# Kernel optimization log

Hardware: AMD Instinct MI355X
Metric: run time of the kernel (lower is better)

Reference implementation:

```python
import jax, jax.numpy as jnp
import numpy as np

B, S, T, H, NH, NL = 16, 128, 64, 128, 8, 4
DH = H // NH
FF = 2 * H
SCALE = 1.0 / float(np.sqrt(DH))


def _ln(x, s, b):
    m = x.mean(-1, keepdims=True)
    v = ((x - m) ** 2).mean(-1, keepdims=True)
    return (x - m) * jax.lax.rsqrt(v + 1e-5) * s + b


def _block(x, mask, p):
    Wq, bq, Wk, bk, Wv, bv, Wo, bo, s1, c1, W1, d1, W2, d2, s2, c2 = p
    N, L, _ = x.shape
    q = (x @ Wq + bq).reshape(N, L, NH, DH)
    k = (x @ Wk + bk).reshape(N, L, NH, DH)
    v = (x @ Wv + bv).reshape(N, L, NH, DH)
    scores = jnp.einsum('nqhd,nkhd->nhqk', q, k) * SCALE
    scores = jnp.where(mask[:, None, :, :], scores, -1e9)
    a = jax.nn.softmax(scores, axis=-1)
    o = jnp.einsum('nhqk,nkhd->nqhd', a, v).reshape(N, L, H)
    x = _ln(x + o @ Wo + bo, s1, c1)
    h = jax.nn.relu(x @ W1 + d1)
    return _ln(x + h @ W2 + d2, s2, c2)


def setup_inputs():
    key = jax.random.key(0)
    ks = jax.random.split(key, 16)
    g = lambda k, shape: jax.random.normal(k, shape, jnp.float32) * 0.02
    return {
        'polylines': jax.random.normal(ks[0], (B, S, T, H), jnp.float32),
        'lengths': jax.random.randint(ks[1], (B, S), 0, T + 1),
        'proj_w': g(ks[2], (H, H)), 'proj_b': jnp.zeros((H,), jnp.float32),
        'proj_ln_s': jnp.ones((H,), jnp.float32), 'proj_ln_b': jnp.zeros((H,), jnp.float32),
        'pos_emb': g(ks[3], (1, T, H)),
        'Wq': g(ks[4], (NL, H, H)), 'bq': jnp.zeros((NL, H), jnp.float32),
        'Wk': g(ks[5], (NL, H, H)), 'bk': jnp.zeros((NL, H), jnp.float32),
        'Wv': g(ks[6], (NL, H, H)), 'bv': jnp.zeros((NL, H), jnp.float32),
        'Wo': g(ks[7], (NL, H, H)), 'bo': jnp.zeros((NL, H), jnp.float32),
        'ln1_s': jnp.ones((NL, H), jnp.float32), 'ln1_b': jnp.zeros((NL, H), jnp.float32),
        'W1': g(ks[8], (NL, H, FF)), 'b1': jnp.zeros((NL, FF), jnp.float32),
        'W2': g(ks[9], (NL, FF, H)), 'b2': jnp.zeros((NL, H), jnp.float32),
        'ln2_s': jnp.ones((NL, H), jnp.float32), 'ln2_b': jnp.zeros((NL, H), jnp.float32),
    }


def reference(polylines, lengths, proj_w, proj_b, proj_ln_s, proj_ln_b, pos_emb,
              Wq, bq, Wk, bk, Wv, bv, Wo, bo, ln1_s, ln1_b, W1, b1, W2, b2, ln2_s, ln2_b):
    # valid[b,s,t] = t < lengths[b,s]; lengths==0 -> polyline absent (fully padded)
    valid = jnp.arange(T)[None, None, :] < lengths[:, :, None]  # [B,S,T]
    x = jnp.where(valid[..., None], polylines, -1.0)            # -1 pad as in np.pad(constant_values=-1)
    # mask_temporal[b,s] = outer(valid[b,s], valid[b,s])
    mask_t = (valid[:, :, :, None] & valid[:, :, None, :]).reshape(B * S, T, T)
    # mask_spatial[b,t] = outer(valid[b,:,t], valid[b,:,t])
    vs = jnp.transpose(valid, (0, 2, 1))                        # [B,T,S]
    mask_s = (vs[:, :, :, None] & vs[:, :, None, :]).reshape(B * T, S, S)

    x = x.reshape(B * S, T, H)
    x = jax.nn.relu(_ln(x @ proj_w + proj_b, proj_ln_s, proj_ln_b))  # MLP: Linear->LN->ReLU
    x = x + pos_emb[:, :T, :]

    mask = mask_t
    for i in range(NL):
        if i == NL // 2:
            # switch from temporal to spatial attention: [B*S,T,H] -> [B*T,S,H]
            x = x.reshape(B, S, T, H).transpose(0, 2, 1, 3).reshape(B * T, S, H)
            mask = mask_s
        p = (Wq[i], bq[i], Wk[i], bk[i], Wv[i], bv[i], Wo[i], bo[i],
             ln1_s[i], ln1_b[i], W1[i], b1[i], W2[i], b2[i], ln2_s[i], ln2_b[i])
        x = _block(x, mask, p)
    # faithful to original final reshape (treats [B*T,S,H] buffer as [B,S,T,H])
    return x.reshape(B, S, T, H)[:, 0, :]
```

## Files before the change

kernel.cpp:

```cpp
#include <hip/hip_runtime.h>

typedef short short8 __attribute__((ext_vector_type(8)));
typedef short short4_t __attribute__((ext_vector_type(4)));
typedef float floatx4 __attribute__((ext_vector_type(4)));
typedef unsigned short ushort_t;

#define B_ 16
#define S_ 128
#define T_ 64
#define H_ 128
#define FF_ 256
#define SCALEQK 0.25f

#define OFFP 0
#define OFFQ(l) (16384 + (l) * 65536)
#define OFFK(l) (OFFQ(l) + 16384)
#define OFFV(l) (OFFQ(l) + 32768)
#define OFFO(l) (OFFQ(l) + 49152)
#define OFFW1(l) (278528 + (l) * 65536)
#define OFFW2(l) (OFFW1(l) + 32768)

__device__ __forceinline__ float b2f(ushort_t u) {
    union { unsigned int i; float f; } x; x.i = ((unsigned int)u) << 16; return x.f;
}
__device__ __forceinline__ ushort_t f2b(float f) {
    union { float f; unsigned int i; } x; x.f = f;
    unsigned int r = x.i + 0x7fffu + ((x.i >> 16) & 1u);
    return (ushort_t)(r >> 16);
}
__device__ __forceinline__ int pack2b(float a, float b) {
    return (int)f2b(a) | ((int)f2b(b) << 16);
}

struct WtEnt { const float* src; int N; int K; int nclog2; int dstoff; };
struct WtArgs { WtEnt e[25]; };

__global__ __launch_bounds__(256) void wt_kernel(WtArgs a, ushort_t* __restrict__ dst) {
    WtEnt ent = a.e[blockIdx.x];
    const int tiles_c = ent.N >> 5;
    const int nt = (ent.K >> 5) * tiles_c;
    const int t = blockIdx.y;
    if (t >= nt) return;
    const int tc = t & (tiles_c - 1);
    const int tr = t >> ent.nclog2;
    __shared__ float ld[32 * 33];
    const int tid = threadIdx.x;
#pragma unroll
    for (int i = 0; i < 4; ++i) {
        int e = tid + i * 256;
        int rr = e >> 5, cc = e & 31;
        ld[rr * 33 + cc] = ent.src[(tr * 32 + rr) * ent.N + tc * 32 + cc];
    }
    __syncthreads();
    ushort_t* d = dst + ent.dstoff;
#pragma unroll
    for (int i = 0; i < 4; ++i) {
        int e = tid + i * 256;
        int rr = e >> 5, cc = e & 31;
        d[(tc * 32 + rr) * ent.K + tr * 32 + cc] = f2b(ld[cc * 33 + rr]);
    }
}

template<int RT, int CT, int KK>
__device__ __forceinline__ void mm_g(const ushort_t* aL, int sa,
                                     const ushort_t* __restrict__ wT,
                                     int colbase, int lane, floatx4 (&acc)[RT][CT]) {
    const int l15 = lane & 15, lq8 = (lane >> 4) * 8;
#pragma unroll
    for (int r = 0; r < RT; ++r)
#pragma unroll
        for (int c = 0; c < CT; ++c) acc[r][c] = (floatx4){0.f, 0.f, 0.f, 0.f};
#pragma unroll
    for (int k0 = 0; k0 < KK; k0 += 32) {
        short8 b[CT];
#pragma unroll
        for (int c = 0; c < CT; ++c)
            b[c] = *(const short8*)&wT[(colbase + c * 16 + l15) * KK + k0 + lq8];
#pragma unroll
        for (int r = 0; r < RT; ++r) {
            short8 a = *(const short8*)&aL[(r * 16 + l15) * sa + k0 + lq8];
#pragma unroll
            for (int c = 0; c < CT; ++c)
                acc[r][c] = __builtin_amdgcn_mfma_f32_16x16x32_bf16(a, b[c], acc[r][c], 0, 0, 0);
        }
    }
}

template<int RT, int CT>
__device__ __forceinline__ void add_bias(floatx4 (&acc)[RT][CT], const float* b,
                                         int colbase, int l15) {
#pragma unroll
    for (int c = 0; c < CT; ++c) {
        float bc = b[colbase + c * 16 + l15];
#pragma unroll
        for (int r = 0; r < RT; ++r)
#pragma unroll
            for (int g = 0; g < 4; ++g) acc[r][c][g] += bc;
    }
}

template<int RT, int CT>
__device__ __forceinline__ void add_resid_reg(floatx4 (&acc)[RT][CT],
                                              const float (&res)[RT][CT][4]) {
#pragma unroll
    for (int r = 0; r < RT; ++r)
#pragma unroll
        for (int c = 0; c < CT; ++c)
#pragma unroll
            for (int g = 0; g < 4; ++g) acc[r][c][g] += res[r][c][g];
}
template<int RT, int CT>
__device__ __forceinline__ void save_resid(float (&res)[RT][CT][4],
                                           const floatx4 (&acc)[RT][CT]) {
#pragma unroll
    for (int r = 0; r < RT; ++r)
#pragma unroll
        for (int c = 0; c < CT; ++c)
#pragma unroll
            for (int g = 0; g < 4; ++g) res[r][c][g] = acc[r][c][g];
}

template<int RT, int CT>
__device__ __forceinline__ void st_n(const floatx4 (&acc)[RT][CT], ushort_t* dst, int stride,
                                     int colbase, int l15, int lq) {
#pragma unroll
    for (int r = 0; r < RT; ++r)
#pragma unroll
        for (int g = 0; g < 4; ++g) {
            int row = r * 16 + lq * 4 + g;
#pragma unroll
            for (int c = 0; c < CT; ++c)
                dst[row * stride + colbase + c * 16 + l15] = f2b(acc[r][c][g]);
        }
}

template<int RT, int CT>
__device__ __forceinline__ void st_t(const floatx4 (&acc)[RT][CT], ushort_t* dst, int stride,
                                     int colbase, int l15, int lq) {
#pragma unroll
    for (int r = 0; r < RT; ++r)
#pragma unroll
        for (int c = 0; c < CT; ++c) {
            int d = colbase + c * 16 + l15;
            short4_t p;
#pragma unroll
            for (int g = 0; g < 4; ++g) p[g] = (short)f2b(acc[r][c][g]);
            *(short4_t*)&dst[d * stride + r * 16 + lq * 4] = p;
        }
}

template<int RT, int CT>
__device__ __forceinline__ void ln_norm(floatx4 (&acc)[RT][CT], float* redL,
                                        const float* lns, const float* lnb,
                                        int colbase, int l15, int lq, int wv) {
#pragma unroll
    for (int r = 0; r < RT; ++r)
#pragma unroll
        for (int g = 0; g < 4; ++g) {
            float s = 0.f, q = 0.f;
#pragma unroll
            for (int c = 0; c < CT; ++c) { float v = acc[r][c][g]; s += v; q += v * v; }
            s += __shfl_xor(s, 1); s += __shfl_xor(s, 2); s += __shfl_xor(s, 4); s += __shfl_xor(s, 8);
            q += __shfl_xor(q, 1); q += __shfl_xor(q, 2); q += __shfl_xor(q, 4); q += __shfl_xor(q, 8);
            if (l15 == 0) {
                int row = r * 16 + lq * 4 + g;
                redL[row * 8 + wv] = s;
                redL[row * 8 + 4 + wv] = q;
            }
        }
    __syncthreads();
#pragma unroll
    for (int r = 0; r < RT; ++r)
#pragma unroll
        for (int g = 0; g < 4; ++g) {
            int row = r * 16 + lq * 4 + g;
            float4 S = *(float4*)&redL[row * 8];
            float4 Q = *(float4*)&redL[row * 8 + 4];
            float mean = (S.x + S.y + S.z + S.w) * (1.f / 128.f);
            float var = (Q.x + Q.y + Q.z + Q.w) * (1.f / 128.f) - mean * mean;
            float rstd = rsqrtf(var + 1e-5f);
#pragma unroll
            for (int c = 0; c < CT; ++c) {
                int col = colbase + c * 16 + l15;
                acc[r][c][g] = (acc[r][c][g] - mean) * rstd * lns[col] + lnb[col];
            }
        }
}

template<int JT>
__device__ __forceinline__ void softmax_pack(floatx4 (&st)[JT], bool iv, unsigned jm,
                                             int (&px)[JT][2]) {
    float ev[JT][4];
    float mx = -3.0e38f;
#pragma unroll
    for (int jt = 0; jt < JT; ++jt)
#pragma unroll
        for (int g = 0; g < 4; ++g) {
            bool ok = iv && ((jm >> (jt * 4 + g)) & 1u);
            float s = ok ? st[jt][g] * SCALEQK : -1e9f;
            ev[jt][g] = s; mx = fmaxf(mx, s);
        }
    mx = fmaxf(mx, __shfl_xor(mx, 16)); mx = fmaxf(mx, __shfl_xor(mx, 32));
    float sum = 0.f;
#pragma unroll
    for (int jt = 0; jt < JT; ++jt)
#pragma unroll
        for (int g = 0; g < 4; ++g) { float e = __expf(ev[jt][g] - mx); ev[jt][g] = e; sum += e; }
    sum += __shfl_xor(sum, 16); sum += __shfl_xor(sum, 32);
    float inv = 1.f / sum;
#pragma unroll
    for (int jt = 0; jt < JT; ++jt) {
        px[jt][0] = pack2b(ev[jt][0] * inv, ev[jt][1] * inv);
        px[jt][1] = pack2b(ev[jt][2] * inv, ev[jt][3] * inv);
    }
}

__device__ __forceinline__ short8 pfrag(const int (*px)[2], int jc, int lq, int l15) {
    const int jA = (lq & 1) * 32 + l15;
    int a0 = __shfl(px[jc * 2][0], jA);
    int a1 = __shfl(px[jc * 2][1], jA);
    int a2 = __shfl(px[jc * 2][0], jA + 16);
    int a3 = __shfl(px[jc * 2][1], jA + 16);
    int b0 = __shfl(px[jc * 2 + 1][0], jA);
    int b1 = __shfl(px[jc * 2 + 1][1], jA);
    int b2 = __shfl(px[jc * 2 + 1][0], jA + 16);
    int b3 = __shfl(px[jc * 2 + 1][1], jA + 16);
    const bool t = (lq >> 1) != 0;
    union { int4 i; short8 s; } u;
    u.i = make_int4(t ? b0 : a0, t ? b1 : a1, t ? b2 : a2, t ? b3 : a3);
    return u.s;
}
__device__ __forceinline__ short8 vfrag(const ushort_t* vT, int stride, int row, int off) {
    int2 a = *(const int2*)&vT[row * stride + off];
    int2 b = *(const int2*)&vT[row * stride + off + 4];
    union { int4 i; short8 s; } u;
    u.i = make_int4(a.x, a.y, b.x, b.y);
    return u.s;
}

__global__ __launch_bounds__(256, 2) void k1_mega(
    const float* __restrict__ poly, const int* __restrict__ lens,
    const ushort_t* __restrict__ wt,
    const float* __restrict__ projb, const float* __restrict__ pls,
    const float* __restrict__ plb, const float* __restrict__ pos,
    const float* __restrict__ bq0, const float* __restrict__ bk0,
    const float* __restrict__ bv0, const float* __restrict__ bo0,
    const float* __restrict__ l1s0, const float* __restrict__ l1b0,
    const float* __restrict__ b10, const float* __restrict__ b20,
    const float* __restrict__ l2s0, const float* __restrict__ l2b0,
    const float* __restrict__ bq1, const float* __restrict__ bk1,
    const float* __restrict__ bv1,
    ushort_t* __restrict__ o1, float* __restrict__ xr0f)
{
    __shared__ ushort_t pool[34816];
    __shared__ float redL[512];
    __shared__ float psL[8 * 68];
    __shared__ float q1L[128];
    ushort_t* xL = pool;
    ushort_t* qL = pool + 8704;
    ushort_t* kL = pool + 17408;
    ushort_t* vT = pool + 26112;
    ushort_t* hL = pool + 17408;

    const int tid = threadIdx.x, lane = tid & 63, wv = tid >> 6;
    const int l15 = lane & 15, lq = lane >> 4;
    const int g = blockIdx.x;
    const int len = lens[g];

    {
        const float* pg = poly + (size_t)g * 8192;
#pragma unroll
        for (int it = 0; it < 8; ++it) {
            int e4 = (tid + it * 256) * 4;
            int row = e4 >> 7, col = e4 & 127;
            float4 f = *(const float4*)(pg + e4);
            if (row >= len) { f.x = -1.f; f.y = -1.f; f.z = -1.f; f.w = -1.f; }
            short4_t u;
            u[0] = (short)f2b(f.x); u[1] = (short)f2b(f.y);
            u[2] = (short)f2b(f.z); u[3] = (short)f2b(f.w);
            *(short4_t*)&xL[row * 136 + col] = u;
        }
    }
    __syncthreads();

    floatx4 a2[4][2];
    float xre[4][2][4];

    mm_g<4, 2, 128>(xL, 136, wt + OFFP, wv * 32, lane, a2);
    add_bias<4, 2>(a2, projb, wv * 32, l15);
    ln_norm<4, 2>(a2, redL, pls, plb, wv * 32, l15, lq, wv);
    __syncthreads();
#pragma unroll
    for (int r = 0; r < 4; ++r)
#pragma unroll
        for (int gg = 0; gg < 4; ++gg) {
            int row = r * 16 + lq * 4 + gg;
#pragma unroll
            for (int c = 0; c < 2; ++c) {
                int col = wv * 32 + c * 16 + l15;
                float v = fmaxf(a2[r][c][gg], 0.f) + pos[row * 128 + col];
                xre[r][c][gg] = v;
                xL[row * 136 + col] = f2b(v);
            }
        }
    __syncthreads();

    mm_g<4, 2, 128>(xL, 136, wt + OFFQ(0), wv * 32, lane, a2);
    add_bias<4, 2>(a2, bq0, wv * 32, l15);
    st_n<4, 2>(a2, qL, 136, wv * 32, l15, lq);
    mm_g<4, 2, 128>(xL, 136, wt + OFFK(0), wv * 32, lane, a2);
    add_bias<4, 2>(a2, bk0, wv * 32, l15);
    st_n<4, 2>(a2, kL, 136, wv * 32, l15, lq);
    mm_g<4, 2, 128>(xL, 136, wt + OFFV(0), wv * 32, lane, a2);
    add_bias<4, 2>(a2, bv0, wv * 32, l15);
    st_t<4, 2>(a2, vT, 68, wv * 32, l15, lq);
    __syncthreads();

    {
        const int iRow = wv * 16 + l15;
        const bool iv = iRow < len;
        unsigned jm = 0;
#pragma unroll
        for (int jt = 0; jt < 4; ++jt)
#pragma unroll
            for (int gg = 0; gg < 4; ++gg)
                if (jt * 16 + lq * 4 + gg < len) jm |= (1u << (jt * 4 + gg));
        for (int h = 0; h < 8; ++h) {
            const int hc = h * 16;
            short8 z8 = {0, 0, 0, 0, 0, 0, 0, 0};
            short8 bqf = z8;
            if (lq < 2) bqf = *(const short8*)&qL[iRow * 136 + hc + lq * 8];
            floatx4 st[4];
#pragma unroll
            for (int jt = 0; jt < 4; ++jt) {
                short8 ak = z8;
                if (lq < 2) ak = *(const short8*)&kL[(jt * 16 + l15) * 136 + hc + lq * 8];
                floatx4 zz = {0.f, 0.f, 0.f, 0.f};
                st[jt] = __builtin_amdgcn_mfma_f32_16x16x32_bf16(ak, bqf, zz, 0, 0, 0);
            }
            int px[4][2];
            softmax_pack<4>(st, iv, jm, px);
            floatx4 ao = {0.f, 0.f, 0.f, 0.f};
#pragma unroll
            for (int jc = 0; jc < 2; ++jc) {
                short8 av = vfrag(vT, 68, hc + l15, jc * 32 + lq * 8);
                short8 bp = pfrag(px, jc, lq, l15);
                ao = __builtin_amdgcn_mfma_f32_16x16x32_bf16(av, bp, ao, 0, 0, 0);
            }
            short4_t w;
#pragma unroll
            for (int gg = 0; gg < 4; ++gg) w[gg] = (short)f2b(ao[gg]);
            *(short4_t*)&qL[iRow * 136 + hc + lq * 4] = w;
        }
    }
    __syncthreads();

    mm_g<4, 2, 128>(qL, 136, wt + OFFO(0), wv * 32, lane, a2);
    add_bias<4, 2>(a2, bo0, wv * 32, l15);
    add_resid_reg<4, 2>(a2, xre);
    ln_norm<4, 2>(a2, redL, l1s0, l1b0, wv * 32, l15, lq, wv);
    save_resid<4, 2>(xre, a2);
    st_n<4, 2>(a2, xL, 136, wv * 32, l15, lq);
    __syncthreads();

    {
        floatx4 a4[4][4];
        mm_g<4, 4, 128>(xL, 136, wt + OFFW1(0), wv * 64, lane, a4);
        add_bias<4, 4>(a4, b10, wv * 64, l15);
#pragma unroll
        for (int r = 0; r < 4; ++r)
#pragma unroll
            for (int c = 0; c < 4; ++c)
#pragma unroll
                for (int gg = 0; gg < 4; ++gg) a4[r][c][gg] = fmaxf(a4[r][c][gg], 0.f);
        st_n<4, 4>(a4, hL, 272, wv * 64, l15, lq);
    }
    __syncthreads();

    mm_g<4, 2, 256>(hL, 272, wt + OFFW2(0), wv * 32, lane, a2);
    add_bias<4, 2>(a2, b20, wv * 32, l15);
    add_resid_reg<4, 2>(a2, xre);
    ln_norm<4, 2>(a2, redL, l2s0, l2b0, wv * 32, l15, lq, wv);
    save_resid<4, 2>(xre, a2);
    st_n<4, 2>(a2, xL, 136, wv * 32, l15, lq);
    if (lq == 0) {
#pragma unroll
        for (int c = 0; c < 2; ++c)
            xr0f[(size_t)g * 128 + wv * 32 + c * 16 + l15] = a2[0][c][0];
    }
    __syncthreads();

    mm_g<4, 2, 128>(xL, 136, wt + OFFK(1), wv * 32, lane, a2);
    add_bias<4, 2>(a2, bk1, wv * 32, l15);
    st_n<4, 2>(a2, kL, 136, wv * 32, l15, lq);
    mm_g<4, 2, 128>(xL, 136, wt + OFFV(1), wv * 32, lane, a2);
    add_bias<4, 2>(a2, bv1, wv * 32, l15);
    st_t<4, 2>(a2, vT, 68, wv * 32, l15, lq);
    if (tid < 128) {
        int d = tid;
        float a = bq1[d];
        const ushort_t* wq = wt + OFFQ(1) + d * 128;
#pragma unroll 4
        for (int j0 = 0; j0 < 128; j0 += 8) {
            short8 w8 = *(const short8*)&wq[j0];
            short8 x8 = *(const short8*)&xL[j0];
#pragma unroll
            for (int q = 0; q < 8; ++q)
                a = fmaf(b2f((ushort_t)x8[q]), b2f((ushort_t)w8[q]), a);
        }
        q1L[d] = a;
    }
    __syncthreads();

    {
        int h = tid >> 5, jj = tid & 31;
        int hc = h * 16;
        float s[2];
#pragma unroll
        for (int half = 0; half < 2; ++half) {
            int j = jj + half * 32;
            float a = 0.f;
            short8 k0v = *(const short8*)&kL[j * 136 + hc];
            short8 k1v = *(const short8*)&kL[j * 136 + hc + 8];
#pragma unroll
            for (int q = 0; q < 8; ++q) {
                a = fmaf(q1L[hc + q], b2f((ushort_t)k0v[q]), a);
                a = fmaf(q1L[hc + 8 + q], b2f((ushort_t)k1v[q]), a);
            }
            s[half] = (j < len) ? a * SCALEQK : -1e9f;
        }
        float mx = fmaxf(s[0], s[1]);
#pragma unroll
        for (int d = 1; d < 32; d <<= 1) mx = fmaxf(mx, __shfl_xor(mx, d));
        float e0 = __expf(s[0] - mx), e1 = __expf(s[1] - mx);
        float sum = e0 + e1;
#pragma unroll
        for (int d = 1; d < 32; d <<= 1) sum += __shfl_xor(sum, d);
        float inv = 1.f / sum;
        psL[h * 68 + jj] = e0 * inv;
        psL[h * 68 + jj + 32] = e1 * inv;
    }
    __syncthreads();
    if (tid < 128) {
        int h = tid >> 4, d = tid & 15, hc = h * 16;
        float a = 0.f;
#pragma unroll 4
        for (int j0 = 0; j0 < 64; j0 += 4) {
            float4 p4 = *(const float4*)&psL[h * 68 + j0];
            short4_t v4 = *(const short4_t*)&vT[(hc + d) * 68 + j0];
            a += p4.x * b2f((ushort_t)v4[0]) + p4.y * b2f((ushort_t)v4[1])
               + p4.z * b2f((ushort_t)v4[2]) + p4.w * b2f((ushort_t)v4[3]);
        }
        o1[(size_t)g * 128 + hc + d] = f2b(a);
    }
}

__global__ __launch_bounds__(256, 1) void k2_tail(
    const int* __restrict__ lens, const ushort_t* __restrict__ wt,
    const ushort_t* __restrict__ o1, const float* __restrict__ xr0f,
    const float* __restrict__ bq, const float* __restrict__ bk,
    const float* __restrict__ bv, const float* __restrict__ bo,
    const float* __restrict__ l1s, const float* __restrict__ l1b,
    const float* __restrict__ b1, const float* __restrict__ b2,
    const float* __restrict__ l2s, const float* __restrict__ l2b,
    float* __restrict__ outp)
{
    __shared__ ushort_t pool[69632];
    __shared__ float redL[1024];
    __shared__ int vld[128];
    ushort_t* yL = pool;
    ushort_t* qL = pool + 17408;
    ushort_t* kL = pool + 34816;
    ushort_t* vT = pool + 52224;
    ushort_t* hL = pool + 34816;

    const int tid = threadIdx.x, lane = tid & 63, wv = tid >> 6;
    const int l15 = lane & 15, lq = lane >> 4;
    const int b = blockIdx.x;

    if (tid < 128) vld[tid] = (lens[b * 128 + tid] > 0) ? 1 : 0;
#pragma unroll
    for (int it = 0; it < 8; ++it) {
        int e = tid + it * 256;
        int row = e >> 4, cg = e & 15;
        *(short8*)&kL[row * 136 + cg * 8] =
            *(const short8*)&o1[((size_t)b * 128 + row) * 128 + cg * 8];
    }
    __syncthreads();

    floatx4 a2[8][2];
    float yre[8][2][4];

    mm_g<8, 2, 128>(kL, 136, wt + OFFO(1), wv * 32, lane, a2);
    add_bias<8, 2>(a2, bo + 128, wv * 32, l15);
#pragma unroll
    for (int r = 0; r < 8; ++r)
#pragma unroll
        for (int gg = 0; gg < 4; ++gg) {
            int row = r * 16 + lq * 4 + gg;
#pragma unroll
            for (int c = 0; c < 2; ++c)
                a2[r][c][gg] += xr0f[((size_t)b * 128 + row) * 128 + wv * 32 + c * 16 + l15];
        }
    ln_norm<8, 2>(a2, redL, l1s + 128, l1b + 128, wv * 32, l15, lq, wv);
    save_resid<8, 2>(yre, a2);
    st_n<8, 2>(a2, yL, 136, wv * 32, l15, lq);
    __syncthreads();
    {
        floatx4 a4[8][4];
        mm_g<8, 4, 128>(yL, 136, wt + OFFW1(1), wv * 64, lane, a4);
        add_bias<8, 4>(a4, b1 + FF_, wv * 64, l15);
#pragma unroll
        for (int r = 0; r < 8; ++r)
#pragma unroll
            for (int c = 0; c < 4; ++c)
#pragma unroll
                for (int gg = 0; gg < 4; ++gg) a4[r][c][gg] = fmaxf(a4[r][c][gg], 0.f);
        st_n<8, 4>(a4, hL, 272, wv * 64, l15, lq);
    }
    __syncthreads();
    mm_g<8, 2, 256>(hL, 272, wt + OFFW2(1), wv * 32, lane, a2);
    add_bias<8, 2>(a2, b2 + 128, wv * 32, l15);
    add_resid_reg<8, 2>(a2, yre);
    ln_norm<8, 2>(a2, redL, l2s + 128, l2b + 128, wv * 32, l15, lq, wv);
    save_resid<8, 2>(yre, a2);
    st_n<8, 2>(a2, yL, 136, wv * 32, l15, lq);
    __syncthreads();

    unsigned jm = 0;
#pragma unroll
    for (int jt = 0; jt < 8; ++jt)
#pragma unroll
        for (int gg = 0; gg < 4; ++gg)
            if (vld[jt * 16 + lq * 4 + gg]) jm |= (1u << (jt * 4 + gg));
    const int i0 = wv * 32 + l15, i1 = i0 + 16;
    const bool iv0 = vld[i0] != 0, iv1 = vld[i1] != 0;

    for (int l = 2; l < 4; ++l) {
        mm_g<8, 2, 128>(yL, 136, wt + OFFQ(l), wv * 32, lane, a2);
        add_bias<8, 2>(a2, bq + l * 128, wv * 32, l15);
        st_n<8, 2>(a2, qL, 136, wv * 32, l15, lq);
        mm_g<8, 2, 128>(yL, 136, wt + OFFK(l), wv * 32, lane, a2);
        add_bias<8, 2>(a2, bk + l * 128, wv * 32, l15);
        st_n<8, 2>(a2, kL, 136, wv * 32, l15, lq);
        mm_g<8, 2, 128>(yL, 136, wt + OFFV(l), wv * 32, lane, a2);
        add_bias<8, 2>(a2, bv + l * 128, wv * 32, l15);
        st_t<8, 2>(a2, vT, 136, wv * 32, l15, lq);
        __syncthreads();
        for (int h = 0; h < 8; ++h) {
            const int hc = h * 16;
            short8 z8 = {0, 0, 0, 0, 0, 0, 0, 0};
            short8 bqa = z8, bqb = z8;
            if (lq < 2) {
                bqa = *(const short8*)&qL[i0 * 136 + hc + lq * 8];
                bqb = *(const short8*)&qL[i1 * 136 + hc + lq * 8];
            }
            floatx4 s0[8], s1[8];
#pragma unroll
            for (int jt = 0; jt < 8; ++jt) {
                short8 ak = z8;
                if (lq < 2) ak = *(const short8*)&kL[(jt * 16 + l15) * 136 + hc + lq * 8];
                floatx4 zz = {0.f, 0.f, 0.f, 0.f};
                s0[jt] = __builtin_amdgcn_mfma_f32_16x16x32_bf16(ak, bqa, zz, 0, 0, 0);
                s1[jt] = __builtin_amdgcn_mfma_f32_16x16x32_bf16(ak, bqb, zz, 0, 0, 0);
            }
            int px0[8][2], px1[8][2];
            softmax_pack<8>(s0, iv0, jm, px0);
            softmax_pack<8>(s1, iv1, jm, px1);
            floatx4 o0 = {0.f, 0.f, 0.f, 0.f}, o1a = {0.f, 0.f, 0.f, 0.f};
#pragma unroll
            for (int jc = 0; jc < 4; ++jc) {
                short8 av = vfrag(vT, 136, hc + l15, jc * 32 + lq * 8);
                o0 = __builtin_amdgcn_mfma_f32_16x16x32_bf16(av, pfrag(px0, jc, lq, l15), o0, 0, 0, 0);
                o1a = __builtin_amdgcn_mfma_f32_16x16x32_bf16(av, pfrag(px1, jc, lq, l15), o1a, 0, 0, 0);
            }
            short4_t w0, w1;
#pragma unroll
            for (int gg = 0; gg < 4; ++gg) { w0[gg] = (short)f2b(o0[gg]); w1[gg] = (short)f2b(o1a[gg]); }
            *(short4_t*)&qL[i0 * 136 + hc + lq * 4] = w0;
            *(short4_t*)&qL[i1 * 136 + hc + lq * 4] = w1;
        }
        __syncthreads();
        mm_g<8, 2, 128>(qL, 136, wt + OFFO(l), wv * 32, lane, a2);
        add_bias<8, 2>(a2, bo + l * 128, wv * 32, l15);
        add_resid_reg<8, 2>(a2, yre);
        ln_norm<8, 2>(a2, redL, l1s + l * 128, l1b + l * 128, wv * 32, l15, lq, wv);
        save_resid<8, 2>(yre, a2);
        st_n<8, 2>(a2, yL, 136, wv * 32, l15, lq);
        __syncthreads();
        {
            floatx4 a4[8][4];
            mm_g<8, 4, 128>(yL, 136, wt + OFFW1(l), wv * 64, lane, a4);
            add_bias<8, 4>(a4, b1 + l * FF_, wv * 64, l15);
#pragma unroll
            for (int r = 0; r < 8; ++r)
#pragma unroll
                for (int c = 0; c < 4; ++c)
#pragma unroll
                    for (int gg = 0; gg < 4; ++gg) a4[r][c][gg] = fmaxf(a4[r][c][gg], 0.f);
            st_n<8, 4>(a4, hL, 272, wv * 64, l15, lq);
        }
        __syncthreads();
        mm_g<8, 2, 256>(hL, 272, wt + OFFW2(l), wv * 32, lane, a2);
        add_bias<8, 2>(a2, b2 + l * 128, wv * 32, l15);
        add_resid_reg<8, 2>(a2, yre);
        ln_norm<8, 2>(a2, redL, l2s + l * 128, l2b + l * 128, wv * 32, l15, lq, wv);
        if (l == 3) {
#pragma unroll
            for (int r = 0; r < 4; ++r)
#pragma unroll
                for (int gg = 0; gg < 4; ++gg) {
                    int row = r * 16 + lq * 4 + gg;
#pragma unroll
                    for (int c = 0; c < 2; ++c)
                        outp[(size_t)b * 8192 + row * 128 + wv * 32 + c * 16 + l15] = a2[r][c][gg];
                }
        } else {
            save_resid<8, 2>(yre, a2);
            st_n<8, 2>(a2, yL, 136, wv * 32, l15, lq);
        }
        __syncthreads();
    }
}

extern "C" void kernel_launch(void* const* d_in, const int* in_sizes, int n_in,
                              void* d_out, int out_size, void* d_ws, size_t ws_size,
                              hipStream_t stream)
{
    const float* poly   = (const float*)d_in[0];
    const int*   lens   = (const int*)d_in[1];
    const float* proj_w = (const float*)d_in[2];
    const float* proj_b = (const float*)d_in[3];
    const float* pls    = (const float*)d_in[4];
    const float* plb    = (const float*)d_in[5];
    const float* pos    = (const float*)d_in[6];
    const float* Wq = (const float*)d_in[7];
    const float* bq = (const float*)d_in[8];
    const float* Wk = (const float*)d_in[9];
    const float* bk = (const float*)d_in[10];
    const float* Wv = (const float*)d_in[11];
    const float* bv = (const float*)d_in[12];
    const float* Wo = (const float*)d_in[13];
    const float* bo = (const float*)d_in[14];
    const float* l1s = (const float*)d_in[15];
    const float* l1b = (const float*)d_in[16];
    const float* W1 = (const float*)d_in[17];
    const float* b1 = (const float*)d_in[18];
    const float* W2 = (const float*)d_in[19];
    const float* b2 = (const float*)d_in[20];
    const float* l2s = (const float*)d_in[21];
    const float* l2b = (const float*)d_in[22];
    float* outp = (float*)d_out;

    char* base = (char*)d_ws;
    ushort_t* wt    = (ushort_t*)base;
    ushort_t* o1buf = (ushort_t*)(base + 1081344);
    float* xr0f     = (float*)(base + 1605632);

    const int HH = H_ * H_, HF = H_ * FF_;
    WtArgs wa;
    wa.e[0] = {proj_w, 128, 128, 2, OFFP};
    for (int l = 0; l < 4; ++l) {
        wa.e[1 + l * 4 + 0] = {Wq + l * HH, 128, 128, 2, OFFQ(l)};
        wa.e[1 + l * 4 + 1] = {Wk + l * HH, 128, 128, 2, OFFK(l)};
        wa.e[1 + l * 4 + 2] = {Wv + l * HH, 128, 128, 2, OFFV(l)};
        wa.e[1 + l * 4 + 3] = {Wo + l * HH, 128, 128, 2, OFFO(l)};
    }
    for (int l = 0; l < 4; ++l) {
        wa.e[17 + l * 2 + 0] = {W1 + l * HF, 256, 128, 3, OFFW1(l)};
        wa.e[17 + l * 2 + 1] = {W2 + l * HF, 128, 256, 2, OFFW2(l)};
    }
    wt_kernel<<<dim3(25, 32), 256, 0, stream>>>(wa, wt);

    k1_mega<<<dim3(2048), 256, 0, stream>>>(
        poly, lens, wt,
        proj_b, pls, plb, pos,
        bq, bk, bv, bo, l1s, l1b, b1, b2, l2s, l2b,
        bq + H_, bk + H_, bv + H_,
        o1buf, xr0f);

    k2_tail<<<dim3(16), 256, 0, stream>>>(
        lens, wt, o1buf, xr0f,
        bq, bk, bv, bo, l1s, l1b, b1, b2, l2s, l2b,
        outp);
}
```

Before: 471.6 us.

## Split fused spatial-attention tail into separate GEMM and attention kernels

Replaces the single 16-block tail kernel, which ran the remaining spatial transformer layers, with a chain of generic MFMA GEMM kernels and a separate scalar attention kernel. Fused epilogues handle bias, ReLU and residual plus layernorm. The goal is to spread the tail work over more blocks, using column and Q/K/V splits and per-head-pair attention blocks. The cost is many extra launches and global-memory round trips for intermediates, and the attention now runs on scalar FMAs instead of MFMA.

```diff
diff --git a/kernel.cpp b/kernel.cpp
--- a/kernel.cpp
+++ b/kernel.cpp
@@ -11,6 +11,11 @@
 #define H_ 128
 #define FF_ 256
 #define SCALEQK 0.25f
+
+#define EPI_BIAS 0
+#define EPI_RELU 1
+#define EPI_LNRES 2
+#define EPI_PROJ 3
 
 #define OFFP 0
 #define OFFQ(l) (16384 + (l) * 65536)
@@ -59,6 +64,240 @@
         int rr = e >> 5, cc = e & 31;
         d[(tc * 32 + rr) * ent.K + tr * 32 + cc] = f2b(ld[cc * 33 + rr]);
     }
+}
+
+template<int K, int EPI, bool PAD, bool FINAL, bool MULTI, bool OUTB, bool AB16>
+__global__ __launch_bounds__(256, 2) void gemm_mfma(
+    const void* __restrict__ Av, int lda,
+    const ushort_t* wt0, const ushort_t* wt1, const ushort_t* wt2,
+    const float* b0, const float* b1, const float* b2,
+    const float* __restrict__ resid, int rstride,
+    const float* __restrict__ lns, const float* __restrict__ lnb,
+    const float* __restrict__ pos, const int* __restrict__ lens,
+    void* o0, void* o1, void* o2,
+    int Ntot)
+{
+    __shared__ ushort_t aL[128 * 136];
+    __shared__ ushort_t wL[128 * 136];
+
+    const int tid = threadIdx.x;
+    const int lane = tid & 63, wv = tid >> 6;
+    const size_t rowbase = (size_t)blockIdx.x * 128;
+
+    const ushort_t* wT; const float* bias; void* out; int cbase;
+    if (MULTI) {
+        int sel = blockIdx.y;
+        wT = sel == 0 ? wt0 : (sel == 1 ? wt1 : wt2);
+        bias = sel == 0 ? b0 : (sel == 1 ? b1 : b2);
+        out = sel == 0 ? o0 : (sel == 1 ? o1 : o2);
+        cbase = 0;
+    } else {
+        wT = wt0; bias = b0; out = o0; cbase = blockIdx.y * 128;
+    }
+
+    floatx4 acc[2][8];
+#pragma unroll
+    for (int a = 0; a < 2; ++a)
+#pragma unroll
+        for (int c = 0; c < 8; ++c) acc[a][c] = (floatx4){0.f, 0.f, 0.f, 0.f};
+
+    const int arow = wv * 32 + (lane & 15);
+    const int koff = (lane >> 4) * 8;
+
+    for (int kc = 0; kc < K; kc += 128) {
+        if (kc) __syncthreads();
+#pragma unroll
+        for (int it = 0; it < 8; ++it) {
+            int e8 = tid + it * 256;
+            int row = e8 >> 4, kg = e8 & 15;
+            int kk = kc + kg * 8;
+            short8 val;
+            if (AB16) {
+                val = *(const short8*)((const ushort_t*)Av + (size_t)(rowbase + row) * lda + kk);
+            } else {
+                const float* Af = (const float*)Av + (size_t)(rowbase + row) * lda + kk;
+                float f[8];
+                *(float4*)(f) = *(const float4*)(Af);
+                *(float4*)(f + 4) = *(const float4*)(Af + 4);
+                if (PAD) {
+                    int r = (int)(rowbase + row);
+                    if ((r & 63) >= lens[r >> 6]) {
+#pragma unroll
+                        for (int q = 0; q < 8; ++q) f[q] = -1.0f;
+                    }
+                }
+#pragma unroll
+                for (int q = 0; q < 8; ++q) val[q] = (short)f2b(f[q]);
+            }
+            *(short8*)&aL[row * 136 + kg * 8] = val;
+        }
+#pragma unroll
+        for (int it = 0; it < 8; ++it) {
+            int e8 = tid + it * 256;
+            int n = e8 >> 4, kg = e8 & 15;
+            *(short8*)&wL[n * 136 + kg * 8] =
+                *(const short8*)&wT[(size_t)(cbase + n) * K + kc + kg * 8];
+        }
+        __syncthreads();
+#pragma unroll
+        for (int k0 = 0; k0 < 128; k0 += 32) {
+            short8 a0 = *(const short8*)&aL[arow * 136 + k0 + koff];
+            short8 a1 = *(const short8*)&aL[(arow + 16) * 136 + k0 + koff];
+#pragma unroll
+            for (int ct = 0; ct < 8; ++ct) {
+                short8 b = *(const short8*)&wL[(ct * 16 + (lane & 15)) * 136 + k0 + koff];
+                acc[0][ct] = __builtin_amdgcn_mfma_f32_16x16x32_bf16(a0, b, acc[0][ct], 0, 0, 0);
+                acc[1][ct] = __builtin_amdgcn_mfma_f32_16x16x32_bf16(a1, b, acc[1][ct], 0, 0, 0);
+            }
+        }
+    }
+
+    const int col16 = lane & 15;
+    const int rgrp = (lane >> 4) * 4;
+    float bcol[8], lnsc[8], lnbc[8];
+#pragma unroll
+    for (int ct = 0; ct < 8; ++ct) bcol[ct] = bias[cbase + ct * 16 + col16];
+    if (EPI == EPI_LNRES || EPI == EPI_PROJ) {
+#pragma unroll
+        for (int ct = 0; ct < 8; ++ct) {
+            lnsc[ct] = lns[ct * 16 + col16];
+            lnbc[ct] = lnb[ct * 16 + col16];
+        }
+    }
+
+#pragma unroll
+    for (int rt = 0; rt < 2; ++rt) {
+        const int rbase = wv * 32 + rt * 16 + rgrp;
+#pragma unroll
+        for (int ct = 0; ct < 8; ++ct)
+#pragma unroll
+            for (int rg = 0; rg < 4; ++rg) {
+                float v = acc[rt][ct][rg] + bcol[ct];
+                if (EPI == EPI_LNRES)
+                    v += resid[(rowbase + rbase + rg) * (size_t)rstride + ct * 16 + col16];
+                acc[rt][ct][rg] = v;
+            }
+        if (EPI == EPI_LNRES || EPI == EPI_PROJ) {
+            float mean[4], rstd[4];
+#pragma unroll
+            for (int rg = 0; rg < 4; ++rg) {
+                float s = 0.f;
+#pragma unroll
+                for (int ct = 0; ct < 8; ++ct) s += acc[rt][ct][rg];
+                s += __shfl_xor(s, 1); s += __shfl_xor(s, 2);
+                s += __shfl_xor(s, 4); s += __shfl_xor(s, 8);
+                mean[rg] = s * (1.f / 128.f);
+            }
+#pragma unroll
+            for (int rg = 0; rg < 4; ++rg) {
+                float s = 0.f;
+#pragma unroll
+                for (int ct = 0; ct < 8; ++ct) {
+                    float d = acc[rt][ct][rg] - mean[rg];
+                    s += d * d;
+                }
+                s += __shfl_xor(s, 1); s += __shfl_xor(s, 2);
+                s += __shfl_xor(s, 4); s += __shfl_xor(s, 8);
+                rstd[rg] = rsqrtf(s * (1.f / 128.f) + 1e-5f);
+            }
+#pragma unroll
+            for (int ct = 0; ct < 8; ++ct)
+#pragma unroll
+                for (int rg = 0; rg < 4; ++rg)
+                    acc[rt][ct][rg] = (acc[rt][ct][rg] - mean[rg]) * rstd[rg] * lnsc[ct] + lnbc[ct];
+        }
+#pragma unroll
+        for (int ct = 0; ct < 8; ++ct)
+#pragma unroll
+            for (int rg = 0; rg < 4; ++rg) {
+                size_t grow = rowbase + rbase + rg;
+                int col = cbase + ct * 16 + col16;
+                float v = acc[rt][ct][rg];
+                if (EPI == EPI_RELU) v = fmaxf(v, 0.f);
+                if (EPI == EPI_PROJ)
+                    v = fmaxf(v, 0.f) + pos[((int)grow & 63) * H_ + ct * 16 + col16];
+                if (FINAL) {
+                    int b = (int)(grow >> 7), s = (int)(grow & 127);
+                    if (s < T_) ((float*)out)[((size_t)(b * T_ + s)) * H_ + col] = v;
+                } else if (OUTB) {
+                    ((ushort_t*)out)[grow * (size_t)Ntot + col] = f2b(v);
+                } else {
+                    ((float*)out)[grow * (size_t)Ntot + col] = v;
+                }
+            }
+    }
+}
+
+__global__ __launch_bounds__(256, 1) void attn_s(
+    ushort_t* qo, const ushort_t* __restrict__ kk, const ushort_t* __restrict__ vv,
+    const int* __restrict__ lens)
+{
+    __shared__ float kL[128 * 36];
+    __shared__ float vL[128 * 36];
+    __shared__ int vldL[128];
+    const int tid = threadIdx.x;
+    const int b = blockIdx.x, hp = blockIdx.y;
+    const size_t rowg = (size_t)b * 128;
+
+    if (tid < 128) vldL[tid] = (lens[b * 128 + tid] > 0) ? 1 : 0;
+#pragma unroll
+    for (int it = 0; it < 2; ++it) {
+        int e8 = tid + it * 256;
+        int j = e8 >> 2, dg = e8 & 3;
+        short8 k8 = *(const short8*)&kk[(rowg + j) * 128 + hp * 32 + dg * 8];
+        short8 v8 = *(const short8*)&vv[(rowg + j) * 128 + hp * 32 + dg * 8];
+        float* kd = &kL[j * 36 + dg * 8];
+        float* vd = &vL[j * 36 + dg * 8];
+#pragma unroll
+        for (int q = 0; q < 8; ++q) { kd[q] = b2f((ushort_t)k8[q]); vd[q] = b2f((ushort_t)v8[q]); }
+    }
+    __syncthreads();
+
+    const int hl = tid >> 7;
+    const int i = tid & 127;
+    const int hc = hl * 16;
+    const int h = hp * 2 + hl;
+
+    float qf[16];
+    {
+        const short8* qp = (const short8*)&qo[(rowg + i) * 128 + h * 16];
+        short8 q0 = qp[0], q1 = qp[1];
+#pragma unroll
+        for (int q = 0; q < 8; ++q) { qf[q] = b2f((ushort_t)q0[q]); qf[8 + q] = b2f((ushort_t)q1[q]); }
+    }
+
+    float sc[128];
+    const bool iv = vldL[i] != 0;
+#pragma unroll
+    for (int j = 0; j < 128; ++j) {
+        const float* kr = &kL[j * 36 + hc];
+        float s = 0.f;
+#pragma unroll
+        for (int d = 0; d < 16; ++d) s = fmaf(qf[d], kr[d], s);
+        sc[j] = (iv && vldL[j]) ? s * SCALEQK : -1e9f;
+    }
+    float m = -3.0e38f;
+#pragma unroll
+    for (int j = 0; j < 128; ++j) m = fmaxf(m, sc[j]);
+    float sum = 0.f;
+#pragma unroll
+    for (int j = 0; j < 128; ++j) { float e = __expf(sc[j] - m); sc[j] = e; sum += e; }
+    const float inv = 1.0f / sum;
+    float of[16];
+#pragma unroll
+    for (int d = 0; d < 16; ++d) of[d] = 0.f;
+#pragma unroll
+    for (int j = 0; j < 128; ++j) {
+        float p = sc[j] * inv;
+        const float* vr = &vL[j * 36 + hc];
+#pragma unroll
+        for (int d = 0; d < 16; ++d) of[d] = fmaf(p, vr[d], of[d]);
+    }
+    short8 o0v, o1v;
+#pragma unroll
+    for (int q = 0; q < 8; ++q) { o0v[q] = (short)f2b(of[q]); o1v[q] = (short)f2b(of[8 + q]); }
+    short8* op = (short8*)&qo[(rowg + i) * 128 + h * 16];
+    op[0] = o0v; op[1] = o1v;
 }
 
 template<int RT, int CT, int KK>
@@ -264,11 +503,11 @@
 
     const int tid = threadIdx.x, lane = tid & 63, wv = tid >> 6;
     const int l15 = lane & 15, lq = lane >> 4;
-    const int g = blockIdx.x;
-    const int len = lens[g];
+    const int gid = blockIdx.x;
+    const int len = lens[gid];
 
     {
-        const float* pg = poly + (size_t)g * 8192;
+        const float* pg = poly + (size_t)gid * 8192;
 #pragma unroll
         for (int it = 0; it < 8; ++it) {
             int e4 = (tid + it * 256) * 4;
@@ -386,7 +625,7 @@
     if (lq == 0) {
 #pragma unroll
         for (int c = 0; c < 2; ++c)
-            xr0f[(size_t)g * 128 + wv * 32 + c * 16 + l15] = a2[0][c][0];
+            xr0f[(size_t)gid * 128 + wv * 32 + c * 16 + l15] = a2[0][c][0];
     }
     __syncthreads();
 
@@ -451,175 +690,7 @@
             a += p4.x * b2f((ushort_t)v4[0]) + p4.y * b2f((ushort_t)v4[1])
                + p4.z * b2f((ushort_t)v4[2]) + p4.w * b2f((ushort_t)v4[3]);
         }
-        o1[(size_t)g * 128 + hc + d] = f2b(a);
-    }
-}
-
-__global__ __launch_bounds__(256, 1) void k2_tail(
-    const int* __restrict__ lens, const ushort_t* __restrict__ wt,
-    const ushort_t* __restrict__ o1, const float* __restrict__ xr0f,
-    const float* __restrict__ bq, const float* __restrict__ bk,
-    const float* __restrict__ bv, const float* __restrict__ bo,
-    const float* __restrict__ l1s, const float* __restrict__ l1b,
-    const float* __restrict__ b1, const float* __restrict__ b2,
-    const float* __restrict__ l2s, const float* __restrict__ l2b,
-    float* __restrict__ outp)
-{
-    __shared__ ushort_t pool[69632];
-    __shared__ float redL[1024];
-    __shared__ int vld[128];
-    ushort_t* yL = pool;
-    ushort_t* qL = pool + 17408;
-    ushort_t* kL = pool + 34816;
-    ushort_t* vT = pool + 52224;
-    ushort_t* hL = pool + 34816;
-
-    const int tid = threadIdx.x, lane = tid & 63, wv = tid >> 6;
-    const int l15 = lane & 15, lq = lane >> 4;
-    const int b = blockIdx.x;
-
-    if (tid < 128) vld[tid] = (lens[b * 128 + tid] > 0) ? 1 : 0;
-#pragma unroll
-    for (int it = 0; it < 8; ++it) {
-        int e = tid + it * 256;
-        int row = e >> 4, cg = e & 15;
-        *(short8*)&kL[row * 136 + cg * 8] =
-            *(const short8*)&o1[((size_t)b * 128 + row) * 128 + cg * 8];
-    }
-    __syncthreads();
-
-    floatx4 a2[8][2];
-    float yre[8][2][4];
-
-    mm_g<8, 2, 128>(kL, 136, wt + OFFO(1), wv * 32, lane, a2);
-    add_bias<8, 2>(a2, bo + 128, wv * 32, l15);
-#pragma unroll
-    for (int r = 0; r < 8; ++r)
-#pragma unroll
-        for (int gg = 0; gg < 4; ++gg) {
-            int row = r * 16 + lq * 4 + gg;
-#pragma unroll
-            for (int c = 0; c < 2; ++c)
-                a2[r][c][gg] += xr0f[((size_t)b * 128 + row) * 128 + wv * 32 + c * 16 + l15];
-        }
-    ln_norm<8, 2>(a2, redL, l1s + 128, l1b + 128, wv * 32, l15, lq, wv);
-    save_resid<8, 2>(yre, a2);
-    st_n<8, 2>(a2, yL, 136, wv * 32, l15, lq);
-    __syncthreads();
-    {
-        floatx4 a4[8][4];
-        mm_g<8, 4, 128>(yL, 136, wt + OFFW1(1), wv * 64, lane, a4);
-        add_bias<8, 4>(a4, b1 + FF_, wv * 64, l15);
-#pragma unroll
-        for (int r = 0; r < 8; ++r)
-#pragma unroll
-            for (int c = 0; c < 4; ++c)
-#pragma unroll
-                for (int gg = 0; gg < 4; ++gg) a4[r][c][gg] = fmaxf(a4[r][c][gg], 0.f);
-        st_n<8, 4>(a4, hL, 272, wv * 64, l15, lq);
-    }
-    __syncthreads();
-    mm_g<8, 2, 256>(hL, 272, wt + OFFW2(1), wv * 32, lane, a2);
-    add_bias<8, 2>(a2, b2 + 128, wv * 32, l15);
-    add_resid_reg<8, 2>(a2, yre);
-    ln_norm<8, 2>(a2, redL, l2s + 128, l2b + 128, wv * 32, l15, lq, wv);
-    save_resid<8, 2>(yre, a2);
-    st_n<8, 2>(a2, yL, 136, wv * 32, l15, lq);
-    __syncthreads();
-
-    unsigned jm = 0;
-#pragma unroll
-    for (int jt = 0; jt < 8; ++jt)
-#pragma unroll
-        for (int gg = 0; gg < 4; ++gg)
-            if (vld[jt * 16 + lq * 4 + gg]) jm |= (1u << (jt * 4 + gg));
-    const int i0 = wv * 32 + l15, i1 = i0 + 16;
-    const bool iv0 = vld[i0] != 0, iv1 = vld[i1] != 0;
-
-    for (int l = 2; l < 4; ++l) {
-        mm_g<8, 2, 128>(yL, 136, wt + OFFQ(l), wv * 32, lane, a2);
-        add_bias<8, 2>(a2, bq + l * 128, wv * 32, l15);
-        st_n<8, 2>(a2, qL, 136, wv * 32, l15, lq);
-        mm_g<8, 2, 128>(yL, 136, wt + OFFK(l), wv * 32, lane, a2);
-        add_bias<8, 2>(a2, bk + l * 128, wv * 32, l15);
-        st_n<8, 2>(a2, kL, 136, wv * 32, l15, lq);
-        mm_g<8, 2, 128>(yL, 136, wt + OFFV(l), wv * 32, lane, a2);
-        add_bias<8, 2>(a2, bv + l * 128, wv * 32, l15);
-        st_t<8, 2>(a2, vT, 136, wv * 32, l15, lq);
-        __syncthreads();
-        for (int h = 0; h < 8; ++h) {
-            const int hc = h * 16;
-            short8 z8 = {0, 0, 0, 0, 0, 0, 0, 0};
-            short8 bqa = z8, bqb = z8;
-            if (lq < 2) {
-                bqa = *(const short8*)&qL[i0 * 136 + hc + lq * 8];
-                bqb = *(const short8*)&qL[i1 * 136 + hc + lq * 8];
-            }
-            floatx4 s0[8], s1[8];
-#pragma unroll
-            for (int jt = 0; jt < 8; ++jt) {
-                short8 ak = z8;
-                if (lq < 2) ak = *(const short8*)&kL[(jt * 16 + l15) * 136 + hc + lq * 8];
-                floatx4 zz = {0.f, 0.f, 0.f, 0.f};
-                s0[jt] = __builtin_amdgcn_mfma_f32_16x16x32_bf16(ak, bqa, zz, 0, 0, 0);
-                s1[jt] = __builtin_amdgcn_mfma_f32_16x16x32_bf16(ak, bqb, zz, 0, 0, 0);
-            }
-            int px0[8][2], px1[8][2];
-            softmax_pack<8>(s0, iv0, jm, px0);
-            softmax_pack<8>(s1, iv1, jm, px1);
-            floatx4 o0 = {0.f, 0.f, 0.f, 0.f}, o1a = {0.f, 0.f, 0.f, 0.f};
-#pragma unroll
-            for (int jc = 0; jc < 4; ++jc) {
-                short8 av = vfrag(vT, 136, hc + l15, jc * 32 + lq * 8);
-                o0 = __builtin_amdgcn_mfma_f32_16x16x32_bf16(av, pfrag(px0, jc, lq, l15), o0, 0, 0, 0);
-                o1a = __builtin_amdgcn_mfma_f32_16x16x32_bf16(av, pfrag(px1, jc, lq, l15), o1a, 0, 0, 0);
-            }
-            short4_t w0, w1;
-#pragma unroll
-            for (int gg = 0; gg < 4; ++gg) { w0[gg] = (short)f2b(o0[gg]); w1[gg] = (short)f2b(o1a[gg]); }
-            *(short4_t*)&qL[i0 * 136 + hc + lq * 4] = w0;
-            *(short4_t*)&qL[i1 * 136 + hc + lq * 4] = w1;
-        }
-        __syncthreads();
-        mm_g<8, 2, 128>(qL, 136, wt + OFFO(l), wv * 32, lane, a2);
-        add_bias<8, 2>(a2, bo + l * 128, wv * 32, l15);
-        add_resid_reg<8, 2>(a2, yre);
-        ln_norm<8, 2>(a2, redL, l1s + l * 128, l1b + l * 128, wv * 32, l15, lq, wv);
-        save_resid<8, 2>(yre, a2);
-        st_n<8, 2>(a2, yL, 136, wv * 32, l15, lq);
-        __syncthreads();
-        {
-            floatx4 a4[8][4];
-            mm_g<8, 4, 128>(yL, 136, wt + OFFW1(l), wv * 64, lane, a4);
-            add_bias<8, 4>(a4, b1 + l * FF_, wv * 64, l15);
-#pragma unroll
-            for (int r = 0; r < 8; ++r)
-#pragma unroll
-                for (int c = 0; c < 4; ++c)
-#pragma unroll
-                    for (int gg = 0; gg < 4; ++gg) a4[r][c][gg] = fmaxf(a4[r][c][gg], 0.f);
-            st_n<8, 4>(a4, hL, 272, wv * 64, l15, lq);
-        }
-        __syncthreads();
-        mm_g<8, 2, 256>(hL, 272, wt + OFFW2(l), wv * 32, lane, a2);
-        add_bias<8, 2>(a2, b2 + l * 128, wv * 32, l15);
-        add_resid_reg<8, 2>(a2, yre);
-        ln_norm<8, 2>(a2, redL, l2s + l * 128, l2b + l * 128, wv * 32, l15, lq, wv);
-        if (l == 3) {
-#pragma unroll
-            for (int r = 0; r < 4; ++r)
-#pragma unroll
-                for (int gg = 0; gg < 4; ++gg) {
-                    int row = r * 16 + lq * 4 + gg;
-#pragma unroll
-                    for (int c = 0; c < 2; ++c)
-                        outp[(size_t)b * 8192 + row * 128 + wv * 32 + c * 16 + l15] = a2[r][c][gg];
-                }
-        } else {
-            save_resid<8, 2>(yre, a2);
-            st_n<8, 2>(a2, yL, 136, wv * 32, l15, lq);
-        }
-        __syncthreads();
+        o1[(size_t)gid * 128 + hc + d] = f2b(a);
     }
 }
 
@@ -656,6 +727,11 @@
     ushort_t* wt    = (ushort_t*)base;
     ushort_t* o1buf = (ushort_t*)(base + 1081344);
     float* xr0f     = (float*)(base + 1605632);
+    float* ybuf     = (float*)(base + 2654208);
+    ushort_t* hsml  = (ushort_t*)(base + 3702784);
+    ushort_t* q2    = (ushort_t*)(base + 4751360);
+    ushort_t* k2b   = (ushort_t*)(base + 5275648);
+    ushort_t* v2    = (ushort_t*)(base + 5799936);
 
     const int HH = H_ * H_, HF = H_ * FF_;
     WtArgs wa;
@@ -679,8 +755,39 @@
         bq + H_, bk + H_, bv + H_,
         o1buf, xr0f);
 
-    k2_tail<<<dim3(16), 256, 0, stream>>>(
-        lens, wt, o1buf, xr0f,
-        bq, bk, bv, bo, l1s, l1b, b1, b2, l2s, l2b,
-        outp);
-}
+    gemm_mfma<128, EPI_LNRES, false, false, false, false, true><<<dim3(16, 1), 256, 0, stream>>>(
+        o1buf, 128, wt + OFFO(1), wt + OFFO(1), wt + OFFO(1), bo + H_, bo + H_, bo + H_,
+        xr0f, 128, l1s + H_, l1b + H_, nullptr, nullptr, ybuf, ybuf, ybuf, H_);
+    gemm_mfma<128, EPI_RELU, false, false, false, true, false><<<dim3(16, 2), 256, 0, stream>>>(
+        ybuf, 128, wt + OFFW1(1), wt + OFFW1(1), wt + OFFW1(1), b1 + FF_, b1 + FF_, b1 + FF_,
+        nullptr, 0, nullptr, nullptr, nullptr, nullptr, hsml, hsml, hsml, FF_);
+    gemm_mfma<256, EPI_LNRES, false, false, false, false, true><<<dim3(16, 1), 256, 0, stream>>>(
+        hsml, 256, wt + OFFW2(1), wt + OFFW2(1), wt + OFFW2(1), b2 + H_, b2 + H_, b2 + H_,
+        ybuf, 128, l2s + H_, l2b + H_, nullptr, nullptr, ybuf, ybuf, ybuf, H_);
+
+    for (int l = 2; l < 4; ++l) {
+        gemm_mfma<128, EPI_BIAS, false, false, true, true, false><<<dim3(16, 3), 256, 0, stream>>>(
+            ybuf, 128, wt + OFFQ(l), wt + OFFK(l), wt + OFFV(l),
+            bq + l * H_, bk + l * H_, bv + l * H_,
+            nullptr, 0, nullptr, nullptr, nullptr, nullptr, q2, k2b, v2, H_);
+        attn_s<<<dim3(16, 4), 256, 0, stream>>>(q2, k2b, v2, lens);
+        gemm_mfma<128, EPI_LNRES, false, false, false, false, true><<<dim3(16, 1), 256, 0, stream>>>(
+            q2, 128, wt + OFFO(l), wt + OFFO(l), wt + OFFO(l), bo + l * H_, bo + l * H_, bo + l * H_,
+            ybuf, 128, l1s + l * H_, l1b + l * H_, nullptr, nullptr, ybuf, ybuf, ybuf, H_);
+        gemm_mfma<128, EPI_RELU, false, false, false, true, false><<<dim3(16, 2), 256, 0, stream>>>(
+            ybuf, 128, wt + OFFW1(l), wt + OFFW1(l), wt + OFFW1(l),
+            b1 + l * FF_, b1 + l * FF_, b1 + l * FF_,
+            nullptr, 0, nullptr, nullptr, nullptr, nullptr, hsml, hsml, hsml, FF_);
+        if (l < 3) {
+            gemm_mfma<256, EPI_LNRES, false, false, false, false, true><<<dim3(16, 1), 256, 0, stream>>>(
+                hsml, 256, wt + OFFW2(l), wt + OFFW2(l), wt + OFFW2(l),
+                b2 + l * H_, b2 + l * H_, b2 + l * H_,
+                ybuf, 128, l2s + l * H_, l2b + l * H_, nullptr, nullptr, ybuf, ybuf, ybuf, H_);
+        } else {
+            gemm_mfma<256, EPI_LNRES, false, true, false, false, true><<<dim3(16, 1), 256, 0, stream>>>(
+                hsml, 256, wt + OFFW2(l), wt + OFFW2(l), wt + OFFW2(l),
+                b2 + l * H_, b2 + l * H_, b2 + l * H_,
+                ybuf, 128, l2s + l * H_, l2b + l * H_, nullptr, nullptr, outp, outp, outp, H_);
+        }
+    }
+}
```

After: 432.0 us. -8.4%, faster.
